# Optimization experiments

Measured on AMD Instinct MI355X. Metric: run time of the kernel, lower is better.

The kernel has to match this reference:

```python
import jax, jax.numpy as jnp
import numpy as np

DS = 16
NUM_INPUTS = 13
WIDTH = 64
DEPTH = 5
NUM_OUTPUTS = 3
# channels of the per-pixel MLP: input gets 4*log2(ds) cosine coord channels
CH = [NUM_INPUTS + 4 * int(np.log2(DS))] + [WIDTH] * (DEPTH - 1) + [NUM_OUTPUTS]


def _splits():
    biases, weights, idx = [], [], 0
    for l in range(len(CH) - 1):
        nci, nco = CH[l], CH[l + 1]
        biases.append((idx, idx + nco)); idx += nco
        weights.append((idx, idx + nco * nci)); idx += nco * nci
    return biases, weights, idx

BIAS_SPLITS, WEIGHT_SPLITS, NUM_PARAMS = _splits()


def _get_coords(bs, h, w, ds):
    """Cosine positional encoding, 4 channels per octave of ds."""
    two_pi = 2.0 * np.pi
    chans = []
    f = ds
    x = jnp.arange(w, dtype=jnp.float32)
    y = jnp.arange(h, dtype=jnp.float32)
    while f > 1:
        px = two_pi * jnp.remainder(x, f) / f  # [w]
        py = two_pi * jnp.remainder(y, f) / f  # [h]
        xcos = jnp.broadcast_to(jnp.cos(px)[None, None, None, :], (bs, 1, h, w))
        xsin = jnp.broadcast_to(jnp.sin(px)[None, None, None, :], (bs, 1, h, w))
        ycos = jnp.broadcast_to(jnp.cos(py)[None, None, :, None], (bs, 1, h, w))
        ysin = jnp.broadcast_to(jnp.sin(py)[None, None, :, None], (bs, 1, h, w))
        chans += [xcos, xsin, ycos, ysin]
        f //= 2
    return jnp.concatenate(chans, axis=1)  # [bs, 4*log2(ds), h, w]


def setup_inputs() -> dict:
    key = jax.random.key(0)
    k1, k2 = jax.random.split(key)
    bs, h, w = 4, 512, 512
    h_lr, w_lr = h // DS, w // DS
    highres = jax.random.normal(k1, (bs, NUM_INPUTS, h, w), dtype=jnp.float32)
    lr_params = jax.random.normal(k2, (bs, NUM_PARAMS, h_lr, w_lr), dtype=jnp.float32)
    return {"highres": highres, "lr_params": lr_params}


def reference(highres, lr_params):
    k = DS
    bs, _, h, w = highres.shape
    _, _, h_lr, w_lr = lr_params.shape

    coords = _get_coords(bs, h, w, k)
    x = jnp.concatenate([highres, coords], axis=1)  # [bs, nci0, h, w]
    nci0 = x.shape[1]

    # unfold into k*k tiles per low-res pixel: [bs, h_lr, w_lr, k*k, nci0]
    tiles = (x.reshape(bs, nci0, h_lr, k, w_lr, k)
              .transpose(0, 2, 4, 3, 5, 1)
              .reshape(bs, h_lr, w_lr, k * k, nci0))

    out = tiles
    n_layers = len(CH) - 1
    for l in range(n_layers):
        nci, nco = CH[l], CH[l + 1]
        ws, we = WEIGHT_SPLITS[l]
        b0, b1 = BIAS_SPLITS[l]
        w_ = (lr_params[:, ws:we].transpose(0, 2, 3, 1)
              .reshape(bs, h_lr, w_lr, nci, nco))
        b_ = (lr_params[:, b0:b1].transpose(0, 2, 3, 1)
              .reshape(bs, h_lr, w_lr, 1, nco))
        out = jnp.einsum('bhwpi,bhwio->bhwpo', out, w_) + b_
        if l < n_layers - 1:
            out = jnp.where(out >= 0, out, 0.01 * out)  # leaky_relu(0.01)
        else:
            out = jnp.tanh(out)

    # fold tiles back to [bs, num_outputs, h, w]
    out = (out.reshape(bs, h_lr, w_lr, k, k, NUM_OUTPUTS)
            .transpose(0, 5, 1, 3, 2, 4)
            .reshape(bs, NUM_OUTPUTS, h, w))
    return out
```

## Files before the change

### kernel.cpp

```cpp
#include <hip/hip_runtime.h>
#include <math.h>

#define NCH   14595
#define WROW  14600
#define HR_C  13
#define IMG_H 512
#define IMG_W 512
#define BS    4

typedef float f32x8 __attribute__((ext_vector_type(8)));
typedef float f32x2 __attribute__((ext_vector_type(2)));


__global__ __launch_bounds__(256) void transpose_params(const float* __restrict__ lp,
                                                        float* __restrict__ wsT) {
    __shared__ float tile[64][65];
    int bid = blockIdx.x;
    int pt = bid & 15;
    int t  = bid >> 4;
    int ct = t % 229;
    int b  = t / 229;
    int c0 = ct * 64, p0 = pt * 64;
    int tp = threadIdx.x & 63;
    int tr = threadIdx.x >> 6;
#pragma unroll
    for (int s = 0; s < 16; s++) {
        int c = c0 + tr + s * 4;
        if (c < NCH)
            tile[tr + s * 4][tp] = lp[((size_t)b * NCH + c) * 1024 + p0 + tp];
    }
    __syncthreads();
#pragma unroll
    for (int s = 0; s < 16; s++) {
        int p = p0 + tr + s * 4;
        int c = c0 + tp;
        if (c < NCH)
            wsT[((size_t)b * 1024 + p) * WROW + c] = tile[tp][tr + s * 4];
    }
}

__device__ __forceinline__ void block_sync_lds() {
    __builtin_amdgcn_sched_barrier(0);
    asm volatile("s_waitcnt lgkmcnt(0)" ::: "memory");
    __builtin_amdgcn_s_barrier();
    __builtin_amdgcn_sched_barrier(0);
}

template<int NCI, bool USE_WS>
__device__ __forceinline__ void mlp_layer(const float* __restrict__ actT,
                                          const float* __restrict__ wl,
                                          const float* __restrict__ lp_col,
                                          int loff, int o0,
                                          int px0, float acc[2][8]) {
#pragma unroll
    for (int j = 0; j < 8; j++) {
        float bv = USE_WS ? wl[j] : lp_col[(size_t)(loff + o0 + j) << 10];
        acc[0][j] = bv; acc[1][j] = bv;
    }
#pragma unroll 4
    for (int k = 0; k < NCI; k++) {
        f32x2 a = *(const f32x2*)&actT[k * 128 + px0];
        if (USE_WS) {
            f32x8 w = *(const f32x8*)(wl + 64 + (k << 6));
#pragma unroll
            for (int j = 0; j < 8; j++) {
                acc[0][j] = fmaf(a.x, w[j], acc[0][j]);
                acc[1][j] = fmaf(a.y, w[j], acc[1][j]);
            }
        } else {
#pragma unroll
            for (int j = 0; j < 8; j++) {
                float w = lp_col[(size_t)(loff + 64 + (k << 6) + o0 + j) << 10];
                acc[0][j] = fmaf(a.x, w, acc[0][j]);
                acc[1][j] = fmaf(a.y, w, acc[1][j]);
            }
        }
    }
}

template<bool USE_WS>
__global__ __launch_bounds__(512, 8) void asap_main(const float* __restrict__ hr,
                                                    const float* __restrict__ lp,
                                                    const float* __restrict__ wsT,
                                                    float* __restrict__ out) {
    __shared__ __align__(16) float actT[64 * 128];

    int bid0 = blockIdx.x;
    int bid  = ((bid0 & 7) << 10) | (bid0 >> 3);

    int half = bid & 1;
    int x    = (bid >> 1) & 31;
    int y    = (bid >> 6) & 31;
    int b    = bid >> 11;
    int tid  = threadIdx.x;
    int lane = tid & 63;
    int wv   = __builtin_amdgcn_readfirstlane(tid >> 6);
    int pix  = y * 32 + x;

    const float* wrow   = wsT + ((size_t)b * 1024 + pix) * WROW;
    const float* lp_col = lp + (size_t)b * NCH * 1024 + pix;

    {
        int Y0 = y * 16 + half * 8, X0 = x * 16;
        for (int t = tid; t < HR_C * 128; t += 512) {
            int c = t >> 7, p = t & 127;
            int row = p >> 4, kx = p & 15;
            actT[c * 128 + p] =
                hr[(((size_t)b * HR_C + c) * IMG_H + Y0 + row) * IMG_W + X0 + kx];
        }
        if (tid < 128) {
            int p = tid, row = p >> 4, kx = p & 15;
            int kyg = half * 8 + row;
            const float two_pi = 6.28318530717958647692f;
            int f = 16;
#pragma unroll
            for (int fi = 0; fi < 4; fi++) {
                float ax = two_pi * (float)(kx & (f - 1)) / (float)f;
                float ay = two_pi * (float)(kyg & (f - 1)) / (float)f;
                actT[(13 + 4 * fi + 0) * 128 + p] = cosf(ax);
                actT[(13 + 4 * fi + 1) * 128 + p] = sinf(ax);
                actT[(13 + 4 * fi + 2) * 128 + p] = cosf(ay);
                actT[(13 + 4 * fi + 3) * 128 + p] = sinf(ay);
                f >>= 1;
            }
        }
    }
    block_sync_lds();

    int o0  = wv << 3;
    int px0 = lane << 1;
    float acc[2][8];

    auto writeback = [&]() {
#pragma unroll
        for (int j = 0; j < 8; j++) {
            f32x2 v;
            v.x = fmaxf(acc[0][j], 0.01f * acc[0][j]);
            v.y = fmaxf(acc[1][j], 0.01f * acc[1][j]);
            *(f32x2*)&actT[(o0 + j) * 128 + px0] = v;
        }
    };

    const float* wl0 = wrow + 0     + o0;
    const float* wl1 = wrow + 1920  + o0;
    const float* wl2 = wrow + 6080  + o0;
    const float* wl3 = wrow + 10240 + o0;

    mlp_layer<29, USE_WS>(actT, wl0, lp_col, 0,     o0, px0, acc);
    block_sync_lds();
    writeback();
    block_sync_lds();

    mlp_layer<64, USE_WS>(actT, wl1, lp_col, 1920,  o0, px0, acc);
    block_sync_lds();
    writeback();
    block_sync_lds();

    mlp_layer<64, USE_WS>(actT, wl2, lp_col, 6080,  o0, px0, acc);
    block_sync_lds();
    writeback();
    block_sync_lds();

    mlp_layer<64, USE_WS>(actT, wl3, lp_col, 10240, o0, px0, acc);
    block_sync_lds();
    writeback();
    block_sync_lds();

    if (wv < 3) {
        float sA, sB;
        if (USE_WS) {
            float bv = wrow[14400 + wv];
            sA = bv; sB = bv;
#pragma unroll 4
            for (int k = 0; k < 64; k++) {
                f32x2 a = *(const f32x2*)&actT[k * 128 + px0];
                float w = wrow[14403 + k * 3 + wv];
                sA = fmaf(a.x, w, sA);
                sB = fmaf(a.y, w, sB);
            }
        } else {
            float bv = lp_col[(size_t)(14400 + wv) << 10];
            sA = bv; sB = bv;
#pragma unroll 4
            for (int k = 0; k < 64; k++) {
                f32x2 a = *(const f32x2*)&actT[k * 128 + px0];
                float w = lp_col[(size_t)(14403 + k * 3 + wv) << 10];
                sA = fmaf(a.x, w, sA);
                sB = fmaf(a.y, w, sB);
            }
        }
        int row = px0 >> 4, kx = px0 & 15;
        int Y = y * 16 + half * 8 + row, X = x * 16 + kx;
        size_t base = ((size_t)(b * 3 + wv)) * IMG_H * IMG_W + (size_t)Y * IMG_W + X;
        f32x2 o;
        o.x = tanhf(sA);
        o.y = tanhf(sB);
        *(f32x2*)&out[base] = o;
    }
}

extern "C" void kernel_launch(void* const* d_in, const int* in_sizes, int n_in,
                              void* d_out, int out_size, void* d_ws, size_t ws_size,
                              hipStream_t stream) {
    const float* hr = (const float*)d_in[0];
    const float* lp = (const float*)d_in[1];
    float* out = (float*)d_out;
    float* wsT = (float*)d_ws;

    size_t need = (size_t)BS * 1024 * WROW * sizeof(float);
    if (ws_size >= need) {
        transpose_params<<<BS * 229 * 16, 256, 0, stream>>>(lp, wsT);
        asap_main<true><<<8192, 512, 0, stream>>>(hr, lp, wsT, out);
    } else {
        asap_main<false><<<8192, 512, 0, stream>>>(hr, lp, wsT, out);
    }
}
```

Baseline: 598.3 us.

## Halve block to 4 waves, each computing 16 output channels per thread

Drops the block from 512 to 256 threads, so each wave computes 16 output channels per pixel pair instead of 8. This doubles the FMAs per LDS activation load and halves the redundant LDS reads across waves. Weights now come through per-lane vector pointers (an asm barrier keeps them in VGPRs) rather than scalar-uniform addresses. The final 3-channel layer is restructured so 128 threads each compute all three outputs for one pixel. The cost is more accumulator registers and fewer waves per block, which can lower occupancy or latency hiding.

After: 1.085 ms. +81.4%, slower.

```diff
diff --git a/kernel.cpp b/kernel.cpp
--- a/kernel.cpp
+++ b/kernel.cpp
@@ -8,8 +8,8 @@
 #define IMG_W 512
 #define BS    4
 
-typedef float f32x8 __attribute__((ext_vector_type(8)));
 typedef float f32x2 __attribute__((ext_vector_type(2)));
+typedef float f32x4 __attribute__((ext_vector_type(4)));
 
 
 __global__ __launch_bounds__(256) void transpose_params(const float* __restrict__ lp,
@@ -46,40 +46,70 @@
     __builtin_amdgcn_sched_barrier(0);
 }
 
-template<int NCI, bool USE_WS>
-__device__ __forceinline__ void mlp_layer(const float* __restrict__ actT,
-                                          const float* __restrict__ wl,
-                                          const float* __restrict__ lp_col,
-                                          int loff, int o0,
-                                          int px0, float acc[2][8]) {
-#pragma unroll
-    for (int j = 0; j < 8; j++) {
-        float bv = USE_WS ? wl[j] : lp_col[(size_t)(loff + o0 + j) << 10];
-        acc[0][j] = bv; acc[1][j] = bv;
-    }
+template<int NCI>
+__device__ __forceinline__ void layer_ws(const float* __restrict__ actT,
+                                         const float* __restrict__ wop,
+                                         int lstart, int o0,
+                                         int px0, float acc[2][16]) {
+    {
+        f32x4 b0 = *(const f32x4*)(wop + lstart + o0);
+        f32x4 b1 = *(const f32x4*)(wop + lstart + o0 + 4);
+        f32x4 b2 = *(const f32x4*)(wop + lstart + o0 + 8);
+        f32x4 b3 = *(const f32x4*)(wop + lstart + o0 + 12);
+#pragma unroll
+        for (int j = 0; j < 4; j++) {
+            acc[0][j]      = b0[j]; acc[1][j]      = b0[j];
+            acc[0][4 + j]  = b1[j]; acc[1][4 + j]  = b1[j];
+            acc[0][8 + j]  = b2[j]; acc[1][8 + j]  = b2[j];
+            acc[0][12 + j] = b3[j]; acc[1][12 + j] = b3[j];
+        }
+    }
+    const float* wk = wop + lstart + 64 + o0;
 #pragma unroll 4
     for (int k = 0; k < NCI; k++) {
+        f32x2 a  = *(const f32x2*)&actT[k * 128 + px0];
+        f32x4 w0 = *(const f32x4*)(wk + (k << 6));
+        f32x4 w1 = *(const f32x4*)(wk + (k << 6) + 4);
+        f32x4 w2 = *(const f32x4*)(wk + (k << 6) + 8);
+        f32x4 w3 = *(const f32x4*)(wk + (k << 6) + 12);
+#pragma unroll
+        for (int j = 0; j < 4; j++) {
+            acc[0][j]      = fmaf(a.x, w0[j], acc[0][j]);
+            acc[1][j]      = fmaf(a.y, w0[j], acc[1][j]);
+            acc[0][4 + j]  = fmaf(a.x, w1[j], acc[0][4 + j]);
+            acc[1][4 + j]  = fmaf(a.y, w1[j], acc[1][4 + j]);
+            acc[0][8 + j]  = fmaf(a.x, w2[j], acc[0][8 + j]);
+            acc[1][8 + j]  = fmaf(a.y, w2[j], acc[1][8 + j]);
+            acc[0][12 + j] = fmaf(a.x, w3[j], acc[0][12 + j]);
+            acc[1][12 + j] = fmaf(a.y, w3[j], acc[1][12 + j]);
+        }
+    }
+}
+
+template<int NCI>
+__device__ __forceinline__ void mlp_layer_slow(const float* __restrict__ actT,
+                                               const float* __restrict__ lp_col,
+                                               int loff, int o0,
+                                               int px0, float acc[2][16]) {
+#pragma unroll
+    for (int j = 0; j < 16; j++) {
+        float bv = lp_col[(size_t)(loff + o0 + j) << 10];
+        acc[0][j] = bv; acc[1][j] = bv;
+    }
+#pragma unroll 2
+    for (int k = 0; k < NCI; k++) {
         f32x2 a = *(const f32x2*)&actT[k * 128 + px0];
-        if (USE_WS) {
-            f32x8 w = *(const f32x8*)(wl + 64 + (k << 6));
-#pragma unroll
-            for (int j = 0; j < 8; j++) {
-                acc[0][j] = fmaf(a.x, w[j], acc[0][j]);
-                acc[1][j] = fmaf(a.y, w[j], acc[1][j]);
-            }
-        } else {
-#pragma unroll
-            for (int j = 0; j < 8; j++) {
-                float w = lp_col[(size_t)(loff + 64 + (k << 6) + o0 + j) << 10];
-                acc[0][j] = fmaf(a.x, w, acc[0][j]);
-                acc[1][j] = fmaf(a.y, w, acc[1][j]);
-            }
+#pragma unroll
+        for (int j = 0; j < 16; j++) {
+            float w = lp_col[(size_t)(loff + 64 + (k << 6) + o0 + j) << 10];
+            acc[0][j] = fmaf(a.x, w, acc[0][j]);
+            acc[1][j] = fmaf(a.y, w, acc[1][j]);
         }
     }
 }
 
 template<bool USE_WS>
-__global__ __launch_bounds__(512, 8) void asap_main(const float* __restrict__ hr,
+__global__ __launch_bounds__(256, 4) void asap_main(const float* __restrict__ hr,
                                                     const float* __restrict__ lp,
                                                     const float* __restrict__ wsT,
                                                     float* __restrict__ out) {
@@ -94,15 +124,18 @@
     int b    = bid >> 11;
     int tid  = threadIdx.x;
     int lane = tid & 63;
-    int wv   = __builtin_amdgcn_readfirstlane(tid >> 6);
+    int wv   = tid >> 6;
     int pix  = y * 32 + x;
 
     const float* wrow   = wsT + ((size_t)b * 1024 + pix) * WROW;
     const float* lp_col = lp + (size_t)b * NCH * 1024 + pix;
 
+    const float* wop = wrow;
+    asm("" : "+v"(wop));
+
     {
         int Y0 = y * 16 + half * 8, X0 = x * 16;
-        for (int t = tid; t < HR_C * 128; t += 512) {
+        for (int t = tid; t < HR_C * 128; t += 256) {
             int c = t >> 7, p = t & 127;
             int row = p >> 4, kx = p & 15;
             actT[c * 128 + p] =
@@ -127,13 +160,13 @@
     }
     block_sync_lds();
 
-    int o0  = wv << 3;
+    int o0  = wv << 4;
     int px0 = lane << 1;
-    float acc[2][8];
+    float acc[2][16];
 
     auto writeback = [&]() {
 #pragma unroll
-        for (int j = 0; j < 8; j++) {
+        for (int j = 0; j < 16; j++) {
             f32x2 v;
             v.x = fmaxf(acc[0][j], 0.01f * acc[0][j]);
             v.y = fmaxf(acc[1][j], 0.01f * acc[1][j]);
@@ -141,61 +174,61 @@
         }
     };
 
-    const float* wl0 = wrow + 0     + o0;
-    const float* wl1 = wrow + 1920  + o0;
-    const float* wl2 = wrow + 6080  + o0;
-    const float* wl3 = wrow + 10240 + o0;
-
-    mlp_layer<29, USE_WS>(actT, wl0, lp_col, 0,     o0, px0, acc);
-    block_sync_lds();
-    writeback();
-    block_sync_lds();
-
-    mlp_layer<64, USE_WS>(actT, wl1, lp_col, 1920,  o0, px0, acc);
-    block_sync_lds();
-    writeback();
-    block_sync_lds();
-
-    mlp_layer<64, USE_WS>(actT, wl2, lp_col, 6080,  o0, px0, acc);
-    block_sync_lds();
-    writeback();
-    block_sync_lds();
-
-    mlp_layer<64, USE_WS>(actT, wl3, lp_col, 10240, o0, px0, acc);
-    block_sync_lds();
-    writeback();
-    block_sync_lds();
-
-    if (wv < 3) {
-        float sA, sB;
-        if (USE_WS) {
-            float bv = wrow[14400 + wv];
-            sA = bv; sB = bv;
+    if (USE_WS) {
+        layer_ws<29>(actT, wop, 0, o0, px0, acc);
+        block_sync_lds(); writeback(); block_sync_lds();
+        layer_ws<64>(actT, wop, 1920, o0, px0, acc);
+        block_sync_lds(); writeback(); block_sync_lds();
+        layer_ws<64>(actT, wop, 6080, o0, px0, acc);
+        block_sync_lds(); writeback(); block_sync_lds();
+        layer_ws<64>(actT, wop, 10240, o0, px0, acc);
+        block_sync_lds(); writeback(); block_sync_lds();
+
+        if (tid < 128) {
+            int p = tid;
+            float s0 = wop[14400], s1 = wop[14401], s2 = wop[14402];
 #pragma unroll 4
             for (int k = 0; k < 64; k++) {
-                f32x2 a = *(const f32x2*)&actT[k * 128 + px0];
-                float w = wrow[14403 + k * 3 + wv];
-                sA = fmaf(a.x, w, sA);
-                sB = fmaf(a.y, w, sB);
+                float a = actT[k * 128 + p];
+                s0 = fmaf(a, wop[14403 + k * 3 + 0], s0);
+                s1 = fmaf(a, wop[14403 + k * 3 + 1], s1);
+                s2 = fmaf(a, wop[14403 + k * 3 + 2], s2);
             }
-        } else {
-            float bv = lp_col[(size_t)(14400 + wv) << 10];
-            sA = bv; sB = bv;
+            int row = p >> 4, kx = p & 15;
+            int Y = y * 16 + half * 8 + row, X = x * 16 + kx;
+            size_t base = ((size_t)b * 3) * IMG_H * IMG_W + (size_t)Y * IMG_W + X;
+            out[base]                             = tanhf(s0);
+            out[base + (size_t)IMG_H * IMG_W]     = tanhf(s1);
+            out[base + (size_t)2 * IMG_H * IMG_W] = tanhf(s2);
+        }
+    } else {
+        mlp_layer_slow<29>(actT, lp_col, 0,     o0, px0, acc);
+        block_sync_lds(); writeback(); block_sync_lds();
+        mlp_layer_slow<64>(actT, lp_col, 1920,  o0, px0, acc);
+        block_sync_lds(); writeback(); block_sync_lds();
+        mlp_layer_slow<64>(actT, lp_col, 6080,  o0, px0, acc);
+        block_sync_lds(); writeback(); block_sync_lds();
+        mlp_layer_slow<64>(actT, lp_col, 10240, o0, px0, acc);
+        block_sync_lds(); writeback(); block_sync_lds();
+        if (tid < 128) {
+            int p = tid;
+            float s0 = lp_col[(size_t)14400 << 10];
+            float s1 = lp_col[(size_t)14401 << 10];
+            float s2 = lp_col[(size_t)14402 << 10];
 #pragma unroll 4
             for (int k = 0; k < 64; k++) {
-                f32x2 a = *(const f32x2*)&actT[k * 128 + px0];
-                float w = lp_col[(size_t)(14403 + k * 3 + wv) << 10];
-                sA = fmaf(a.x, w, sA);
-                sB = fmaf(a.y, w, sB);
+                float a = actT[k * 128 + p];
+                s0 = fmaf(a, lp_col[(size_t)(14403 + k * 3 + 0) << 10], s0);
+                s1 = fmaf(a, lp_col[(size_t)(14403 + k * 3 + 1) << 10], s1);
+                s2 = fmaf(a, lp_col[(size_t)(14403 + k * 3 + 2) << 10], s2);
             }
-        }
-        int row = px0 >> 4, kx = px0 & 15;
-        int Y = y * 16 + half * 8 + row, X = x * 16 + kx;
-        size_t base = ((size_t)(b * 3 + wv)) * IMG_H * IMG_W + (size_t)Y * IMG_W + X;
-        f32x2 o;
-        o.x = tanhf(sA);
-        o.y = tanhf(sB);
-        *(f32x2*)&out[base] = o;
+            int row = p >> 4, kx = p & 15;
+            int Y = y * 16 + half * 8 + row, X = x * 16 + kx;
+            size_t base = ((size_t)b * 3) * IMG_H * IMG_W + (size_t)Y * IMG_W + X;
+            out[base]                             = tanhf(s0);
+            out[base + (size_t)IMG_H * IMG_W]     = tanhf(s1);
+            out[base + (size_t)2 * IMG_H * IMG_W] = tanhf(s2);
+        }
     }
 }
 
@@ -210,8 +243,8 @@
     size_t need = (size_t)BS * 1024 * WROW * sizeof(float);
     if (ws_size >= need) {
         transpose_params<<<BS * 229 * 16, 256, 0, stream>>>(lp, wsT);
-        asap_main<true><<<8192, 512, 0, stream>>>(hr, lp, wsT, out);
+        asap_main<true><<<8192, 256, 0, stream>>>(hr, lp, wsT, out);
     } else {
-        asap_main<false><<<8192, 512, 0, stream>>>(hr, lp, wsT, out);
-    }
-}
+        asap_main<false><<<8192, 256, 0, stream>>>(hr, lp, wsT, out);
+    }
+}
```
